# Kernel tuning notes

Measured on AMD Instinct MI355X. Metric: run time of the kernel, lower is better.

## Reference

```python
import jax, jax.numpy as jnp
import numpy as np

B, T, C, H = 32, 500, 256, 8  # batch, seq, n_embd(=in_c), heads


def setup_inputs() -> dict:
    key = jax.random.key(0)
    ks = jax.random.split(key, 6)
    s = 0.02
    return {
        "x": jax.random.normal(ks[0], (B, T, C), dtype=jnp.float32),
        # nn.Linear(in_c, 3*n_embd): store as [in, out] for x @ W
        "W_attn": jax.random.normal(ks[1], (C, 3 * C), dtype=jnp.float32) * s,
        "b_attn": jnp.zeros((3 * C,), dtype=jnp.float32),
        # nn.Conv1d(heads, 1, 1, bias=False): a per-head mixing weight [H]
        "p_w": jax.random.normal(ks[2], (H,), dtype=jnp.float32) * s,
        # nn.Linear(n_embd, n_embd)
        "W_proj": jax.random.normal(ks[3], (C, C), dtype=jnp.float32) * s,
        "b_proj": jnp.zeros((C,), dtype=jnp.float32),
    }


def reference(x, W_attn, b_attn, p_w, W_proj, b_proj):
    Bx, Tx, Cx = x.shape
    Hh = p_w.shape[0]
    d = Cx // Hh
    qkv = x @ W_attn + b_attn                          # [B,T,3C]
    q, k, v = jnp.split(qkv, 3, axis=-1)
    # [B,T,C] -> [B,H,T,d]
    q = q.reshape(Bx, Tx, Hh, d).transpose(0, 2, 1, 3)
    k = k.reshape(Bx, Tx, Hh, d).transpose(0, 2, 1, 3)
    v = v.reshape(Bx, Tx, Hh, d).transpose(0, 2, 1, 3)
    scale = 1.0 / np.sqrt(d).astype(np.float32)
    att = jnp.einsum('bhtd,bhsd->bhts', q, k) * scale  # [B,H,T,T]
    # bias buffer is all ones for T<=500, so masked_fill is a no-op
    # pred path: 1x1 conv over heads (weighted sum), then sigmoid
    pred_weight = jax.nn.sigmoid(jnp.einsum('bhts,h->bts', att, p_w))  # [B,T,T]
    pred_weight = jnp.where(jnp.isnan(pred_weight), 0.0, pred_weight)
    # value path: softmax @ V
    a = jax.nn.softmax(att, axis=-1)                   # [B,H,T,T]
    ctx = jnp.einsum('bhts,bhsd->bhtd', a, v)          # [B,H,T,d]
    ctx = ctx.transpose(0, 2, 1, 3).reshape(Bx, Tx, Cx)  # [B,T,C]
    value = ctx @ W_proj + b_proj
    return (pred_weight, value)
```

## Files before the change

kernel.cpp:

```cpp
#include <hip/hip_runtime.h>
#include <stddef.h>

typedef unsigned short u16;
typedef unsigned int u32;
typedef __attribute__((ext_vector_type(4))) float f32x4;
typedef __attribute__((ext_vector_type(8))) u16 u16x8;
typedef __attribute__((ext_vector_type(4))) u16 u16x4;
typedef __attribute__((ext_vector_type(8))) short s16x8;
typedef __attribute__((ext_vector_type(2))) u32 u32x2;
typedef __attribute__((ext_vector_type(4))) u32 u32x4;

#define MFMA16 __builtin_amdgcn_mfma_f32_16x16x32_bf16

__device__ __forceinline__ float bf2f(u16 u) { return __uint_as_float(((u32)u) << 16); }
__device__ __forceinline__ u16 f2bf(float f) {
  u32 u = __float_as_uint(f);
  return (u16)((u + 0x7FFFu + ((u >> 16) & 1u)) >> 16);
}
__device__ __forceinline__ u32 cvt_pk_bf16(float lo, float hi) {
  u32 r; asm("v_cvt_pk_bf16_f32 %0, %1, %2" : "=v"(r) : "v"(lo), "v"(hi)); return r;
}

union frag_u { u32x4 u; s16x8 s; };


__global__ __launch_bounds__(256) void transpose_w(
    const float* __restrict__ W, u16* __restrict__ Wt, int K, int N)
{
  __shared__ u16 T[64][72];
  const int tid = threadIdx.x;
  const int k0 = blockIdx.x * 64, n0 = blockIdx.y * 64;
#pragma unroll
  for (int it = 0; it < 4; ++it) {
    const int r = it * 16 + (tid >> 4);
    const int c = (tid & 15) * 4;
    f32x4 v = *(const f32x4*)&W[(size_t)(k0 + r) * N + n0 + c];
    u16x4 o;
    o[0] = f2bf(v[0]); o[1] = f2bf(v[1]); o[2] = f2bf(v[2]); o[3] = f2bf(v[3]);
    *(u16x4*)&T[r][c] = o;
  }
  __syncthreads();
#pragma unroll
  for (int it = 0; it < 4; ++it) {
    const int n = it * 16 + (tid >> 4);
    const int kc = (tid & 15) * 4;
    u16x4 o;
    o[0] = T[kc + 0][n]; o[1] = T[kc + 1][n];
    o[2] = T[kc + 2][n]; o[3] = T[kc + 3][n];
    *(u16x4*)&Wt[(size_t)(n0 + n) * K + k0 + kc] = o;
  }
}

__global__ __launch_bounds__(512, 2) void gemm_qkv(
    const float* __restrict__ x, const u16* __restrict__ WtA,
    const float* __restrict__ bias, u16* __restrict__ qkbuf, u16* __restrict__ vt)
{
  __shared__ u16 As[64][264];
  const int tid = threadIdx.x;
  const int lane = tid & 63;
  const int w = tid >> 6;
  const int cl = lane & 15, g = lane >> 4;
  const int wm = w >> 2, wn = w & 3;
  const int m0 = blockIdx.x * 64;

#pragma unroll
  for (int it = 0; it < 4; ++it) {
    const int ci = tid + it * 512;
    const int row = ci >> 5;
    const int c8 = (ci & 31) * 8;
    f32x4 lo = *(const f32x4*)&x[(size_t)(m0 + row) * 256 + c8];
    f32x4 hi = *(const f32x4*)&x[(size_t)(m0 + row) * 256 + c8 + 4];
    u32x4 p;
    p[0] = cvt_pk_bf16(lo[0], lo[1]); p[1] = cvt_pk_bf16(lo[2], lo[3]);
    p[2] = cvt_pk_bf16(hi[0], hi[1]); p[3] = cvt_pk_bf16(hi[2], hi[3]);
    *(u32x4*)&As[row][c8] = p;
  }
  __syncthreads();

  s16x8 af[2][8];
#pragma unroll
  for (int mi = 0; mi < 2; ++mi)
#pragma unroll
    for (int kt = 0; kt < 8; ++kt)
      af[mi][kt] = *(const s16x8*)&As[wm * 32 + mi * 16 + cl][kt * 32 + g * 8];

#pragma unroll 1
  for (int nc = 0; nc < 3; ++nc) {
    const int n0 = wn * 192 + nc * 64;
    f32x4 acc[2][4];
#pragma unroll
    for (int mi = 0; mi < 2; ++mi)
#pragma unroll
      for (int ni = 0; ni < 4; ++ni) acc[mi][ni] = (f32x4){0.f, 0.f, 0.f, 0.f};
#pragma unroll
    for (int kt = 0; kt < 8; ++kt) {
      s16x8 bf[4];
#pragma unroll
      for (int ni = 0; ni < 4; ++ni)
        bf[ni] = *(const s16x8*)&WtA[(size_t)(n0 + ni * 16 + cl) * 256 + kt * 32 + g * 8];
#pragma unroll
      for (int mi = 0; mi < 2; ++mi)
#pragma unroll
        for (int ni = 0; ni < 4; ++ni)
          acc[mi][ni] = MFMA16(af[mi][kt], bf[ni], acc[mi][ni], 0, 0, 0);
    }
    float bb[4];
#pragma unroll
    for (int ni = 0; ni < 4; ++ni) bb[ni] = bias[n0 + ni * 16 + cl];
    if (n0 < 512) {
#pragma unroll
      for (int mi = 0; mi < 2; ++mi)
#pragma unroll
        for (int ni = 0; ni < 4; ++ni)
#pragma unroll
          for (int r = 0; r < 4; ++r) {
            const int m = m0 + wm * 32 + mi * 16 + g * 4 + r;
            qkbuf[(size_t)m * 512 + n0 + ni * 16 + cl] = f2bf(acc[mi][ni][r] + bb[ni]);
          }
    } else {
#pragma unroll
      for (int mi = 0; mi < 2; ++mi)
#pragma unroll
        for (int ni = 0; ni < 4; ++ni) {
          const int cb = n0 - 512 + ni * 16 + cl;
#pragma unroll
          for (int r = 0; r < 4; ++r) {
            const int m = m0 + wm * 32 + mi * 16 + g * 4 + r;
            const int b2 = m / 500;
            const int t2 = m - b2 * 500;
            vt[(size_t)(b2 * 256 + cb) * 500 + t2] = f2bf(acc[mi][ni][r] + bb[ni]);
          }
        }
    }
  }
}

__global__ __launch_bounds__(256) void pred_gemm(
    const u16* __restrict__ qk, const float* __restrict__ pw_g,
    float* __restrict__ pred)
{
  const int tid = threadIdx.x;
  const int lane = tid & 63;
  const int w = tid >> 6;
  const int cl = lane & 15, g = lane >> 4;
  const int lin = blockIdx.x;
  const int xcd = lin & 7, idx = lin >> 3;
  const int b = xcd * 4 + (idx >> 4);
  const int tile = idx & 15;
  const int tm = tile >> 2, tn = tile & 3;
  const int r0 = tm * 128 + (w >> 1) * 64;
  const int c0 = tn * 128 + (w & 1) * 64;
  const float scale = 0.17677669529663687f;

  const u16* qkb = qk + (size_t)b * 500 * 512;
  float fw[8];
#pragma unroll
  for (int h = 0; h < 8; ++h) fw[h] = pw_g[h] * scale;

  f32x4 acc[4][4];
#pragma unroll
  for (int mi = 0; mi < 4; ++mi)
#pragma unroll
    for (int ni = 0; ni < 4; ++ni) acc[mi][ni] = (f32x4){0.f, 0.f, 0.f, 0.f};

#pragma unroll 2
  for (int kt = 0; kt < 8; ++kt) {
    const int k0 = kt * 32;
    s16x8 af[4], bf[4];
#pragma unroll
    for (int mi = 0; mi < 4; ++mi) {
      int t = r0 + mi * 16 + cl; if (t > 499) t = 499;
      af[mi] = *(const s16x8*)&qkb[(size_t)t * 512 + k0 + g * 8];
    }
#pragma unroll
    for (int ni = 0; ni < 4; ++ni) {
      int s = c0 + ni * 16 + cl; if (s > 499) s = 499;
      bf[ni] = *(const s16x8*)&qkb[(size_t)s * 512 + 256 + k0 + g * 8];
    }
    const f32x4 zf = (f32x4){0.f, 0.f, 0.f, 0.f};
    const float f = fw[kt];
#pragma unroll
    for (int mi = 0; mi < 4; ++mi)
#pragma unroll
      for (int ni = 0; ni < 4; ++ni) {
        f32x4 part = MFMA16(af[mi], bf[ni], zf, 0, 0, 0);
#pragma unroll
        for (int r = 0; r < 4; ++r) acc[mi][ni][r] = fmaf(f, part[r], acc[mi][ni][r]);
      }
  }
#pragma unroll
  for (int mi = 0; mi < 4; ++mi)
#pragma unroll
    for (int ni = 0; ni < 4; ++ni) {
      const int s = c0 + ni * 16 + cl;
#pragma unroll
      for (int r = 0; r < 4; ++r) {
        const int t = r0 + mi * 16 + g * 4 + r;
        if (t < 500 && s < 500) {
          pred[(size_t)(b * 500 + t) * 500 + s] =
              1.f / (1.f + __expf(-acc[mi][ni][r]));
        }
      }
    }
}

__global__ __launch_bounds__(256) void attn_value(
    const u16* __restrict__ qk, const u16* __restrict__ vt, u16* __restrict__ ctx)
{
  const int tid = threadIdx.x;
  const int w = tid >> 6;
  const int lane = tid & 63;
  const int cl = lane & 15, g = lane >> 4;
  const int lin = blockIdx.x;
  const int xcd = lin & 7, idx = lin >> 3;
  const int b = xcd * 4 + (idx >> 5);
  const int rem = idx & 31;
  const int h = rem >> 2, qg = rem & 3;
  const int t0 = qg * 128 + w * 32;
  const float scale = 0.17677669529663687f;

  const u16* qkb = qk + (size_t)b * 500 * 512;
  const u16* vtb = vt + (size_t)b * 256 * 500;

  s16x8 qf[2];
#pragma unroll
  for (int qi = 0; qi < 2; ++qi) {
    int tq = t0 + qi * 16 + cl; if (tq > 499) tq = 499;
    qf[qi] = *(const s16x8*)&qkb[(size_t)tq * 512 + h * 32 + g * 8];
  }
  f32x4 of[2][2];
  float lsum[2] = {0.f, 0.f};
#pragma unroll
  for (int qi = 0; qi < 2; ++qi) {
    of[qi][0] = (f32x4){0.f, 0.f, 0.f, 0.f};
    of[qi][1] = (f32x4){0.f, 0.f, 0.f, 0.f};
  }
  const int sA = (g & 1) * 32 + cl;
  const int sB = sA + 16;
  const bool hiHalf = (lane >= 32);

#pragma unroll 1
  for (int st = 0; st < 8; ++st) {
    const int s0 = st * 64;
    s16x8 kf[4];
#pragma unroll
    for (int si = 0; si < 4; ++si) {
      int sr = s0 + si * 16 + cl; if (sr > 499) sr = 499;
      kf[si] = *(const s16x8*)&qkb[(size_t)sr * 512 + 256 + h * 32 + g * 8];
    }
    s16x8 vf[2][2];
#pragma unroll
    for (int di = 0; di < 2; ++di)
#pragma unroll
      for (int s32 = 0; s32 < 2; ++s32)
        vf[di][s32] = *(const s16x8*)&vtb[(size_t)(h * 32 + di * 16 + cl) * 500 +
                                          s0 + s32 * 32 + g * 8];
    const f32x4 zf = (f32x4){0.f, 0.f, 0.f, 0.f};
    u32 P2[2][4][2];
#pragma unroll
    for (int qi = 0; qi < 2; ++qi) {
#pragma unroll
      for (int si = 0; si < 4; ++si) {
        f32x4 St = MFMA16(kf[si], qf[qi], zf, 0, 0, 0);
        float pv[4];
#pragma unroll
        for (int r = 0; r < 4; ++r) {
          int sidx = s0 + si * 16 + g * 4 + r;
          float e = __expf(St[r] * scale);
          pv[r] = (sidx < 500) ? e : 0.f;
          lsum[qi] += pv[r];
        }
        P2[qi][si][0] = cvt_pk_bf16(pv[0], pv[1]);
        P2[qi][si][1] = cvt_pk_bf16(pv[2], pv[3]);
      }
    }
#pragma unroll
    for (int s32 = 0; s32 < 2; ++s32) {
#pragma unroll
      for (int qi = 0; qi < 2; ++qi) {
        u32 Z0 = hiHalf ? P2[qi][2 * s32 + 1][0] : P2[qi][2 * s32][0];
        u32 Z1 = hiHalf ? P2[qi][2 * s32 + 1][1] : P2[qi][2 * s32][1];
        frag_u fu;
        fu.u[0] = (u32)__shfl((int)Z0, sA);
        fu.u[1] = (u32)__shfl((int)Z1, sA);
        fu.u[2] = (u32)__shfl((int)Z0, sB);
        fu.u[3] = (u32)__shfl((int)Z1, sB);
        of[qi][0] = MFMA16(fu.s, vf[0][s32], of[qi][0], 0, 0, 0);
        of[qi][1] = MFMA16(fu.s, vf[1][s32], of[qi][1], 0, 0, 0);
      }
    }
  }
#pragma unroll
  for (int qi = 0; qi < 2; ++qi) {
    float l2 = lsum[qi] + __shfl_xor(lsum[qi], 16);
    l2 += __shfl_xor(l2, 32);
#pragma unroll
    for (int r = 0; r < 4; ++r) {
      const int tq = t0 + qi * 16 + g * 4 + r;
      if (tq < 500) {
        const float inv = 1.f / __shfl(l2, g * 4 + r);
        ctx[(size_t)(b * 500 + tq) * 256 + h * 32 + cl]      = f2bf(of[qi][0][r] * inv);
        ctx[(size_t)(b * 500 + tq) * 256 + h * 32 + 16 + cl] = f2bf(of[qi][1][r] * inv);
      }
    }
  }
}

__global__ __launch_bounds__(512, 2) void gemm_proj(
    const u16* __restrict__ ctx, const u16* __restrict__ WtP,
    const float* __restrict__ bias, float* __restrict__ out)
{
  __shared__ u16 As[64][264];
  const int tid = threadIdx.x;
  const int lane = tid & 63;
  const int w = tid >> 6;
  const int cl = lane & 15, g = lane >> 4;
  const int wm = w >> 2, wn = w & 3;
  const int m0 = blockIdx.x * 64;

#pragma unroll
  for (int it = 0; it < 4; ++it) {
    const int ci = tid + it * 512;
    const int row = ci >> 5;
    const int c8 = (ci & 31) * 8;
    *(u32x4*)&As[row][c8] = *(const u32x4*)&ctx[(size_t)(m0 + row) * 256 + c8];
  }
  __syncthreads();

  s16x8 af[2][8];
#pragma unroll
  for (int mi = 0; mi < 2; ++mi)
#pragma unroll
    for (int kt = 0; kt < 8; ++kt)
      af[mi][kt] = *(const s16x8*)&As[wm * 32 + mi * 16 + cl][kt * 32 + g * 8];

  const int n0 = wn * 64;
  f32x4 acc[2][4];
#pragma unroll
  for (int mi = 0; mi < 2; ++mi)
#pragma unroll
    for (int ni = 0; ni < 4; ++ni) acc[mi][ni] = (f32x4){0.f, 0.f, 0.f, 0.f};
#pragma unroll
  for (int kt = 0; kt < 8; ++kt) {
    s16x8 bf[4];
#pragma unroll
    for (int ni = 0; ni < 4; ++ni)
      bf[ni] = *(const s16x8*)&WtP[(size_t)(n0 + ni * 16 + cl) * 256 + kt * 32 + g * 8];
#pragma unroll
    for (int mi = 0; mi < 2; ++mi)
#pragma unroll
      for (int ni = 0; ni < 4; ++ni)
        acc[mi][ni] = MFMA16(af[mi][kt], bf[ni], acc[mi][ni], 0, 0, 0);
  }
  float bb[4];
#pragma unroll
  for (int ni = 0; ni < 4; ++ni) bb[ni] = bias[n0 + ni * 16 + cl];
#pragma unroll
  for (int mi = 0; mi < 2; ++mi)
#pragma unroll
    for (int ni = 0; ni < 4; ++ni)
#pragma unroll
      for (int r = 0; r < 4; ++r) {
        const int m = m0 + wm * 32 + mi * 16 + g * 4 + r;
        out[(size_t)m * 256 + n0 + ni * 16 + cl] = acc[mi][ni][r] + bb[ni];
      }
}

extern "C" void kernel_launch(void* const* d_in, const int* in_sizes, int n_in,
                              void* d_out, int out_size, void* d_ws, size_t ws_size,
                              hipStream_t stream)
{
  const float* x      = (const float*)d_in[0];
  const float* W_attn = (const float*)d_in[1];
  const float* b_attn = (const float*)d_in[2];
  const float* p_w    = (const float*)d_in[3];
  const float* W_proj = (const float*)d_in[4];
  const float* b_proj = (const float*)d_in[5];

  float* pred   = (float*)d_out;
  float* valout = pred + 8000000;

  u16* qkbuf = (u16*)d_ws;
  u16* vt    = (u16*)((char*)d_ws + 16384000);
  u16* ctx   = (u16*)((char*)d_ws + 24576000);
  u16* WtA   = ctx;
  u16* WtP   = qkbuf;

  hipLaunchKernelGGL(transpose_w, dim3(4, 12), dim3(256), 0, stream,
                     W_attn, WtA, 256, 768);
  hipLaunchKernelGGL(gemm_qkv, dim3(250), dim3(512), 0, stream,
                     x, WtA, b_attn, qkbuf, vt);
  hipLaunchKernelGGL(pred_gemm, dim3(512), dim3(256), 0, stream,
                     qkbuf, p_w, pred);
  hipLaunchKernelGGL(attn_value, dim3(1024), dim3(256), 0, stream,
                     qkbuf, vt, ctx);
  hipLaunchKernelGGL(transpose_w, dim3(4, 4), dim3(256), 0, stream,
                     W_proj, WtP, 256, 256);
  hipLaunchKernelGGL(gemm_proj, dim3(250), dim3(512), 0, stream,
                     ctx, WtP, b_proj, valout);
}
```

Baseline: 107.0 us.

## Fuse attention with output projection, merge weight transposes, retile QKV and pred GEMMs

Merges the two weight-transpose launches into one kernel. The attention kernel now runs all 8 heads of a 32-query tile in one 512-thread block, writes the normalized context to shared memory and applies the output projection in place. This removes the ctx round trip through global memory and two launches. The QKV GEMM and the pred GEMM switch to smaller tiles with more blocks and higher occupancy hints, which raises parallelism at the cost of more redundant operand loads.

```diff
diff --git a/kernel.cpp b/kernel.cpp
--- a/kernel.cpp
+++ b/kernel.cpp
@@ -7,12 +7,10 @@
 typedef __attribute__((ext_vector_type(8))) u16 u16x8;
 typedef __attribute__((ext_vector_type(4))) u16 u16x4;
 typedef __attribute__((ext_vector_type(8))) short s16x8;
-typedef __attribute__((ext_vector_type(2))) u32 u32x2;
 typedef __attribute__((ext_vector_type(4))) u32 u32x4;
 
 #define MFMA16 __builtin_amdgcn_mfma_f32_16x16x32_bf16
 
-__device__ __forceinline__ float bf2f(u16 u) { return __uint_as_float(((u32)u) << 16); }
 __device__ __forceinline__ u16 f2bf(float f) {
   u32 u = __float_as_uint(f);
   return (u16)((u + 0x7FFFu + ((u >> 16) & 1u)) >> 16);
@@ -24,12 +22,17 @@
 union frag_u { u32x4 u; s16x8 s; };
 
 
-__global__ __launch_bounds__(256) void transpose_w(
-    const float* __restrict__ W, u16* __restrict__ Wt, int K, int N)
+__global__ __launch_bounds__(256) void transpose_both(
+    const float* __restrict__ Wa, const float* __restrict__ Wp,
+    u16* __restrict__ WtA, u16* __restrict__ WtP)
 {
   __shared__ u16 T[64][72];
   const int tid = threadIdx.x;
-  const int k0 = blockIdx.x * 64, n0 = blockIdx.y * 64;
+  const int yy = blockIdx.y;
+  const float* W; u16* Wt; int N, n0;
+  if (yy < 12) { W = Wa; Wt = WtA; N = 768; n0 = yy * 64; }
+  else         { W = Wp; Wt = WtP; N = 256; n0 = (yy - 12) * 64; }
+  const int k0 = blockIdx.x * 64;
 #pragma unroll
   for (int it = 0; it < 4; ++it) {
     const int r = it * 16 + (tid >> 4);
@@ -47,24 +50,23 @@
     u16x4 o;
     o[0] = T[kc + 0][n]; o[1] = T[kc + 1][n];
     o[2] = T[kc + 2][n]; o[3] = T[kc + 3][n];
-    *(u16x4*)&Wt[(size_t)(n0 + n) * K + k0 + kc] = o;
-  }
-}
-
-__global__ __launch_bounds__(512, 2) void gemm_qkv(
+    *(u16x4*)&Wt[(size_t)(n0 + n) * 256 + k0 + kc] = o;
+  }
+}
+
+__global__ __launch_bounds__(512, 4) void gemm_qkv(
     const float* __restrict__ x, const u16* __restrict__ WtA,
     const float* __restrict__ bias, u16* __restrict__ qkbuf, u16* __restrict__ vt)
 {
-  __shared__ u16 As[64][264];
+  __shared__ u16 As[32][264];
   const int tid = threadIdx.x;
   const int lane = tid & 63;
   const int w = tid >> 6;
   const int cl = lane & 15, g = lane >> 4;
-  const int wm = w >> 2, wn = w & 3;
-  const int m0 = blockIdx.x * 64;
-
-#pragma unroll
-  for (int it = 0; it < 4; ++it) {
+  const int m0 = blockIdx.x * 32;
+
+#pragma unroll
+  for (int it = 0; it < 2; ++it) {
     const int ci = tid + it * 512;
     const int row = ci >> 5;
     const int c8 = (ci & 31) * 8;
@@ -77,65 +79,54 @@
   }
   __syncthreads();
 
-  s16x8 af[2][8];
-#pragma unroll
-  for (int mi = 0; mi < 2; ++mi)
-#pragma unroll
-    for (int kt = 0; kt < 8; ++kt)
-      af[mi][kt] = *(const s16x8*)&As[wm * 32 + mi * 16 + cl][kt * 32 + g * 8];
-
-#pragma unroll 1
-  for (int nc = 0; nc < 3; ++nc) {
-    const int n0 = wn * 192 + nc * 64;
-    f32x4 acc[2][4];
-#pragma unroll
-    for (int mi = 0; mi < 2; ++mi)
-#pragma unroll
-      for (int ni = 0; ni < 4; ++ni) acc[mi][ni] = (f32x4){0.f, 0.f, 0.f, 0.f};
-#pragma unroll
-    for (int kt = 0; kt < 8; ++kt) {
-      s16x8 bf[4];
-#pragma unroll
-      for (int ni = 0; ni < 4; ++ni)
-        bf[ni] = *(const s16x8*)&WtA[(size_t)(n0 + ni * 16 + cl) * 256 + kt * 32 + g * 8];
+  f32x4 acc[2][6];
+#pragma unroll
+  for (int mi = 0; mi < 2; ++mi)
+#pragma unroll
+    for (int nf = 0; nf < 6; ++nf) acc[mi][nf] = (f32x4){0.f, 0.f, 0.f, 0.f};
+
+#pragma unroll
+  for (int kt = 0; kt < 8; ++kt) {
+    s16x8 af0 = *(const s16x8*)&As[cl][kt * 32 + g * 8];
+    s16x8 af1 = *(const s16x8*)&As[16 + cl][kt * 32 + g * 8];
+    s16x8 bf[6];
+#pragma unroll
+    for (int nf = 0; nf < 6; ++nf)
+      bf[nf] = *(const s16x8*)&WtA[(size_t)(w * 96 + nf * 16 + cl) * 256 + kt * 32 + g * 8];
+#pragma unroll
+    for (int nf = 0; nf < 6; ++nf) {
+      acc[0][nf] = MFMA16(af0, bf[nf], acc[0][nf], 0, 0, 0);
+      acc[1][nf] = MFMA16(af1, bf[nf], acc[1][nf], 0, 0, 0);
+    }
+  }
+#pragma unroll
+  for (int nf = 0; nf < 6; ++nf) {
+    const int n = w * 96 + nf * 16;
+    const float bb = bias[n + cl];
+    if (n < 512) {
 #pragma unroll
       for (int mi = 0; mi < 2; ++mi)
 #pragma unroll
-        for (int ni = 0; ni < 4; ++ni)
-          acc[mi][ni] = MFMA16(af[mi][kt], bf[ni], acc[mi][ni], 0, 0, 0);
-    }
-    float bb[4];
-#pragma unroll
-    for (int ni = 0; ni < 4; ++ni) bb[ni] = bias[n0 + ni * 16 + cl];
-    if (n0 < 512) {
+        for (int r = 0; r < 4; ++r) {
+          const int m = m0 + mi * 16 + g * 4 + r;
+          qkbuf[(size_t)m * 512 + n + cl] = f2bf(acc[mi][nf][r] + bb);
+        }
+    } else {
+      const int cb = n - 512 + cl;
 #pragma unroll
       for (int mi = 0; mi < 2; ++mi)
 #pragma unroll
-        for (int ni = 0; ni < 4; ++ni)
-#pragma unroll
-          for (int r = 0; r < 4; ++r) {
-            const int m = m0 + wm * 32 + mi * 16 + g * 4 + r;
-            qkbuf[(size_t)m * 512 + n0 + ni * 16 + cl] = f2bf(acc[mi][ni][r] + bb[ni]);
-          }
-    } else {
-#pragma unroll
-      for (int mi = 0; mi < 2; ++mi)
-#pragma unroll
-        for (int ni = 0; ni < 4; ++ni) {
-          const int cb = n0 - 512 + ni * 16 + cl;
-#pragma unroll
-          for (int r = 0; r < 4; ++r) {
-            const int m = m0 + wm * 32 + mi * 16 + g * 4 + r;
-            const int b2 = m / 500;
-            const int t2 = m - b2 * 500;
-            vt[(size_t)(b2 * 256 + cb) * 500 + t2] = f2bf(acc[mi][ni][r] + bb[ni]);
-          }
+        for (int r = 0; r < 4; ++r) {
+          const int m = m0 + mi * 16 + g * 4 + r;
+          const int b2 = m / 500;
+          const int t2 = m - b2 * 500;
+          vt[(size_t)(b2 * 256 + cb) * 500 + t2] = f2bf(acc[mi][nf][r] + bb);
         }
     }
   }
 }
 
-__global__ __launch_bounds__(256) void pred_gemm(
+__global__ __launch_bounds__(256, 4) void pred_gemm(
     const u16* __restrict__ qk, const float* __restrict__ pw_g,
     float* __restrict__ pred)
 {
@@ -145,11 +136,11 @@
   const int cl = lane & 15, g = lane >> 4;
   const int lin = blockIdx.x;
   const int xcd = lin & 7, idx = lin >> 3;
-  const int b = xcd * 4 + (idx >> 4);
-  const int tile = idx & 15;
-  const int tm = tile >> 2, tn = tile & 3;
-  const int r0 = tm * 128 + (w >> 1) * 64;
-  const int c0 = tn * 128 + (w & 1) * 64;
+  const int b = xcd * 4 + (idx >> 5);
+  const int tile = idx & 31;
+  const int tm = tile >> 3, tn = tile & 7;
+  const int r0 = tm * 128 + w * 32;
+  const int c0 = tn * 64;
   const float scale = 0.17677669529663687f;
 
   const u16* qkb = qk + (size_t)b * 500 * 512;
@@ -157,18 +148,18 @@
 #pragma unroll
   for (int h = 0; h < 8; ++h) fw[h] = pw_g[h] * scale;
 
-  f32x4 acc[4][4];
-#pragma unroll
-  for (int mi = 0; mi < 4; ++mi)
+  f32x4 acc[2][4];
+#pragma unroll
+  for (int mi = 0; mi < 2; ++mi)
 #pragma unroll
     for (int ni = 0; ni < 4; ++ni) acc[mi][ni] = (f32x4){0.f, 0.f, 0.f, 0.f};
 
-#pragma unroll 2
+#pragma unroll
   for (int kt = 0; kt < 8; ++kt) {
     const int k0 = kt * 32;
-    s16x8 af[4], bf[4];
-#pragma unroll
-    for (int mi = 0; mi < 4; ++mi) {
+    s16x8 af[2], bf[4];
+#pragma unroll
+    for (int mi = 0; mi < 2; ++mi) {
       int t = r0 + mi * 16 + cl; if (t > 499) t = 499;
       af[mi] = *(const s16x8*)&qkb[(size_t)t * 512 + k0 + g * 8];
     }
@@ -180,7 +171,7 @@
     const f32x4 zf = (f32x4){0.f, 0.f, 0.f, 0.f};
     const float f = fw[kt];
 #pragma unroll
-    for (int mi = 0; mi < 4; ++mi)
+    for (int mi = 0; mi < 2; ++mi)
 #pragma unroll
       for (int ni = 0; ni < 4; ++ni) {
         f32x4 part = MFMA16(af[mi], bf[ni], zf, 0, 0, 0);
@@ -189,7 +180,7 @@
       }
   }
 #pragma unroll
-  for (int mi = 0; mi < 4; ++mi)
+  for (int mi = 0; mi < 2; ++mi)
 #pragma unroll
     for (int ni = 0; ni < 4; ++ni) {
       const int s = c0 + ni * 16 + cl;
@@ -204,19 +195,20 @@
     }
 }
 
-__global__ __launch_bounds__(256) void attn_value(
-    const u16* __restrict__ qk, const u16* __restrict__ vt, u16* __restrict__ ctx)
-{
+__global__ __launch_bounds__(512, 4) void attn_proj(
+    const u16* __restrict__ qk, const u16* __restrict__ vt,
+    const u16* __restrict__ WtP, const float* __restrict__ bias,
+    float* __restrict__ out)
+{
+  __shared__ u16 ctxs[32][264];
   const int tid = threadIdx.x;
   const int w = tid >> 6;
   const int lane = tid & 63;
   const int cl = lane & 15, g = lane >> 4;
   const int lin = blockIdx.x;
   const int xcd = lin & 7, idx = lin >> 3;
-  const int b = xcd * 4 + (idx >> 5);
-  const int rem = idx & 31;
-  const int h = rem >> 2, qg = rem & 3;
-  const int t0 = qg * 128 + w * 32;
+  const int b = xcd * 4 + (idx >> 4);
+  const int t0 = (idx & 15) * 32;
   const float scale = 0.17677669529663687f;
 
   const u16* qkb = qk + (size_t)b * 500 * 512;
@@ -226,7 +218,7 @@
 #pragma unroll
   for (int qi = 0; qi < 2; ++qi) {
     int tq = t0 + qi * 16 + cl; if (tq > 499) tq = 499;
-    qf[qi] = *(const s16x8*)&qkb[(size_t)tq * 512 + h * 32 + g * 8];
+    qf[qi] = *(const s16x8*)&qkb[(size_t)tq * 512 + w * 32 + g * 8];
   }
   f32x4 of[2][2];
   float lsum[2] = {0.f, 0.f};
@@ -246,14 +238,14 @@
 #pragma unroll
     for (int si = 0; si < 4; ++si) {
       int sr = s0 + si * 16 + cl; if (sr > 499) sr = 499;
-      kf[si] = *(const s16x8*)&qkb[(size_t)sr * 512 + 256 + h * 32 + g * 8];
+      kf[si] = *(const s16x8*)&qkb[(size_t)sr * 512 + 256 + w * 32 + g * 8];
     }
     s16x8 vf[2][2];
 #pragma unroll
     for (int di = 0; di < 2; ++di)
 #pragma unroll
       for (int s32 = 0; s32 < 2; ++s32)
-        vf[di][s32] = *(const s16x8*)&vtb[(size_t)(h * 32 + di * 16 + cl) * 500 +
+        vf[di][s32] = *(const s16x8*)&vtb[(size_t)(w * 32 + di * 16 + cl) * 500 +
                                           s0 + s32 * 32 + g * 8];
     const f32x4 zf = (f32x4){0.f, 0.f, 0.f, 0.f};
     u32 P2[2][4][2];
@@ -296,73 +288,45 @@
     l2 += __shfl_xor(l2, 32);
 #pragma unroll
     for (int r = 0; r < 4; ++r) {
-      const int tq = t0 + qi * 16 + g * 4 + r;
-      if (tq < 500) {
-        const float inv = 1.f / __shfl(l2, g * 4 + r);
-        ctx[(size_t)(b * 500 + tq) * 256 + h * 32 + cl]      = f2bf(of[qi][0][r] * inv);
-        ctx[(size_t)(b * 500 + tq) * 256 + h * 32 + 16 + cl] = f2bf(of[qi][1][r] * inv);
-      }
-    }
-  }
-}
-
-__global__ __launch_bounds__(512, 2) void gemm_proj(
-    const u16* __restrict__ ctx, const u16* __restrict__ WtP,
-    const float* __restrict__ bias, float* __restrict__ out)
-{
-  __shared__ u16 As[64][264];
-  const int tid = threadIdx.x;
-  const int lane = tid & 63;
-  const int w = tid >> 6;
-  const int cl = lane & 15, g = lane >> 4;
-  const int wm = w >> 2, wn = w & 3;
-  const int m0 = blockIdx.x * 64;
-
-#pragma unroll
-  for (int it = 0; it < 4; ++it) {
-    const int ci = tid + it * 512;
-    const int row = ci >> 5;
-    const int c8 = (ci & 31) * 8;
-    *(u32x4*)&As[row][c8] = *(const u32x4*)&ctx[(size_t)(m0 + row) * 256 + c8];
+      const float inv = 1.f / __shfl(l2, g * 4 + r);
+      const int row = qi * 16 + g * 4 + r;
+      ctxs[row][w * 32 + cl]      = f2bf(of[qi][0][r] * inv);
+      ctxs[row][w * 32 + 16 + cl] = f2bf(of[qi][1][r] * inv);
+    }
   }
   __syncthreads();
 
-  s16x8 af[2][8];
-#pragma unroll
-  for (int mi = 0; mi < 2; ++mi)
-#pragma unroll
-    for (int kt = 0; kt < 8; ++kt)
-      af[mi][kt] = *(const s16x8*)&As[wm * 32 + mi * 16 + cl][kt * 32 + g * 8];
-
-  const int n0 = wn * 64;
-  f32x4 acc[2][4];
-#pragma unroll
-  for (int mi = 0; mi < 2; ++mi)
-#pragma unroll
-    for (int ni = 0; ni < 4; ++ni) acc[mi][ni] = (f32x4){0.f, 0.f, 0.f, 0.f};
+  const int n0 = w * 32;
+  f32x4 acc[2][2];
+#pragma unroll
+  for (int mi = 0; mi < 2; ++mi)
+#pragma unroll
+    for (int ni = 0; ni < 2; ++ni) acc[mi][ni] = (f32x4){0.f, 0.f, 0.f, 0.f};
 #pragma unroll
   for (int kt = 0; kt < 8; ++kt) {
-    s16x8 bf[4];
-#pragma unroll
-    for (int ni = 0; ni < 4; ++ni)
+    s16x8 af[2], bf[2];
+#pragma unroll
+    for (int mi = 0; mi < 2; ++mi)
+      af[mi] = *(const s16x8*)&ctxs[mi * 16 + cl][kt * 32 + g * 8];
+#pragma unroll
+    for (int ni = 0; ni < 2; ++ni)
       bf[ni] = *(const s16x8*)&WtP[(size_t)(n0 + ni * 16 + cl) * 256 + kt * 32 + g * 8];
 #pragma unroll
     for (int mi = 0; mi < 2; ++mi)
 #pragma unroll
-      for (int ni = 0; ni < 4; ++ni)
-        acc[mi][ni] = MFMA16(af[mi][kt], bf[ni], acc[mi][ni], 0, 0, 0);
-  }
-  float bb[4];
-#pragma unroll
-  for (int ni = 0; ni < 4; ++ni) bb[ni] = bias[n0 + ni * 16 + cl];
-#pragma unroll
-  for (int mi = 0; mi < 2; ++mi)
-#pragma unroll
-    for (int ni = 0; ni < 4; ++ni)
+      for (int ni = 0; ni < 2; ++ni)
+        acc[mi][ni] = MFMA16(af[mi], bf[ni], acc[mi][ni], 0, 0, 0);
+  }
+  float bb[2] = { bias[n0 + cl], bias[n0 + 16 + cl] };
+#pragma unroll
+  for (int mi = 0; mi < 2; ++mi)
+#pragma unroll
+    for (int ni = 0; ni < 2; ++ni)
 #pragma unroll
       for (int r = 0; r < 4; ++r) {
-        const int m = m0 + wm * 32 + mi * 16 + g * 4 + r;
-        out[(size_t)m * 256 + n0 + ni * 16 + cl] = acc[mi][ni][r] + bb[ni];
+        const int t = t0 + mi * 16 + g * 4 + r;
+        if (t < 500)
+          out[(size_t)(b * 500 + t) * 256 + n0 + ni * 16 + cl] = acc[mi][ni][r] + bb[ni];
       }
 }
 
@@ -382,20 +346,15 @@
 
   u16* qkbuf = (u16*)d_ws;
   u16* vt    = (u16*)((char*)d_ws + 16384000);
-  u16* ctx   = (u16*)((char*)d_ws + 24576000);
-  u16* WtA   = ctx;
-  u16* WtP   = qkbuf;
-
-  hipLaunchKernelGGL(transpose_w, dim3(4, 12), dim3(256), 0, stream,
-                     W_attn, WtA, 256, 768);
-  hipLaunchKernelGGL(gemm_qkv, dim3(250), dim3(512), 0, stream,
+  u16* WtA   = (u16*)((char*)d_ws + 24576000);
+  u16* WtP   = (u16*)((char*)d_ws + 24969216);
+
+  hipLaunchKernelGGL(transpose_both, dim3(4, 16), dim3(256), 0, stream,
+                     W_attn, W_proj, WtA, WtP);
+  hipLaunchKernelGGL(gemm_qkv, dim3(500), dim3(512), 0, stream,
                      x, WtA, b_attn, qkbuf, vt);
-  hipLaunchKernelGGL(pred_gemm, dim3(512), dim3(256), 0, stream,
+  hipLaunchKernelGGL(pred_gemm, dim3(1024), dim3(256), 0, stream,
                      qkbuf, p_w, pred);
-  hipLaunchKernelGGL(attn_value, dim3(1024), dim3(256), 0, stream,
-                     qkbuf, vt, ctx);
-  hipLaunchKernelGGL(transpose_w, dim3(4, 4), dim3(256), 0, stream,
-                     W_proj, WtP, 256, 256);
-  hipLaunchKernelGGL(gemm_proj, dim3(250), dim3(512), 0, stream,
-                     ctx, WtP, b_proj, valout);
-}
+  hipLaunchKernelGGL(attn_proj, dim3(512), dim3(512), 0, stream,
+                     qkbuf, vt, WtP, b_proj, valout);
+}
```

Result: slower. 193.2 us (+80.6%).
